# Optimization experiments

Measured on AMD Instinct MI355X. Metric: run time of the kernel, lower is better.

Reference implementation:

```python
import jax, jax.numpy as jnp
import numpy as np

N = 200000       # nodes
E = 6400000      # edges
F_IN, H1, H2, C = 7, 32, 16, 2


def gcn_conv(x, W, b, src, dst, n):
    """PyG GCNConv: add self-loops, symmetric normalization, linear, scatter-add."""
    loop = jnp.arange(n, dtype=src.dtype)
    s = jnp.concatenate([src, loop])
    d = jnp.concatenate([dst, loop])
    # degree of target nodes (with self-loops)
    deg = jax.ops.segment_sum(jnp.ones_like(d, dtype=x.dtype), d, num_segments=n)
    dinv = jnp.where(deg > 0, jax.lax.rsqrt(deg), 0.0)
    h = x @ W                                  # [n, out]
    norm = dinv[s] * dinv[d]                   # [e+n]
    msg = h[s] * norm[:, None]                 # gather + normalize
    out = jax.ops.segment_sum(msg, d, num_segments=n)  # scatter-add aggregation
    return out + b


def setup_inputs() -> dict:
    key = jax.random.key(0)
    ks = jax.random.split(key, 8)
    x = jax.random.normal(ks[0], (N, F_IN), dtype=jnp.float32)
    edge_index = jax.random.randint(ks[1], (2, E), 0, N, dtype=jnp.int64)
    def glorot(k, fan_in, fan_out):
        lim = np.sqrt(6.0 / (fan_in + fan_out)).astype(np.float32)
        return jax.random.uniform(k, (fan_in, fan_out), jnp.float32, -lim, lim)
    return {
        "x": x,
        "edge_index": edge_index,
        "W1": glorot(ks[2], F_IN, H1), "b1": jnp.zeros((H1,), jnp.float32),
        "W2": glorot(ks[3], H1, H2), "b2": jnp.zeros((H2,), jnp.float32),
        "Wfc": glorot(ks[4], H2, C), "bfc": jnp.zeros((C,), jnp.float32),
    }


def reference(x, edge_index, W1, b1, W2, b2, Wfc, bfc):
    src, dst = edge_index[0], edge_index[1]
    h = jax.nn.relu(gcn_conv(x, W1, b1, src, dst, N))
    h = jax.nn.relu(gcn_conv(h, W2, b2, src, dst, N))
    return h @ Wfc + bfc
```

## Files before the change

kernel.cpp:

```cpp
#include <hip/hip_runtime.h>

#define NNODES 200000
#define NEDGES 6400000
#define FIN 7
#define FH1 32
#define FH2 16
#define NC 2

#define WB 128
#define WB_SHIFT 7
#define NBUCK ((NNODES + WB - 1) / WB)
#define NBLK 512
#define CHUNK (NEDGES / NBLK)
#define PSHIFT 18
#define SRCMASK ((1u << PSHIFT) - 1)

#define RSTRIDE 4608
#define SCAP 5120


__global__ __launch_bounds__(256) void zero_cnt(int* __restrict__ cnt) {
    int i = blockIdx.x * 256 + threadIdx.x;
    if (i < NBUCK) cnt[i] = 0;
}


__global__ __launch_bounds__(256) void p2_sortres(const int* __restrict__ ei,
                                                  int* __restrict__ bucket_cur,
                                                  unsigned int* __restrict__ recs) {
    __shared__ int sorted[CHUNK];
    __shared__ int lcur[NBUCK];
    __shared__ int gbase[NBUCK];
    __shared__ int sm[256];
    int t = threadIdx.x;
    int blk = blockIdx.x;

    for (int i = t; i < NBUCK; i += 256) lcur[i] = 0;
    __syncthreads();

    int ebase = blk * CHUNK;
    for (int e = ebase + t; e < ebase + CHUNK; e += 256)
        atomicAdd(&lcur[ei[NEDGES + e] >> WB_SHIFT], 1);
    __syncthreads();

    int base7 = t * 7;
    int loc[7];
    int s = 0;
#pragma unroll
    for (int k = 0; k < 7; ++k) {
        int idx = base7 + k;
        int v = (idx < NBUCK) ? lcur[idx] : 0;
        loc[k] = v;
        s += v;
    }
    sm[t] = s;
    __syncthreads();
    for (int off = 1; off < 256; off <<= 1) {
        int v = (t >= off) ? sm[t - off] : 0;
        __syncthreads();
        sm[t] += v;
        __syncthreads();
    }
    int run = sm[t] - s;
#pragma unroll
    for (int k = 0; k < 7; ++k) {
        int idx = base7 + k;
        if (idx < NBUCK) { lcur[idx] = run; run += loc[k]; }
    }
    __syncthreads();

    for (int e = ebase + t; e < ebase + CHUNK; e += 256) {
        int src = ei[e];
        int d = ei[NEDGES + e];
        int b = d >> WB_SHIFT;
        int slot = atomicAdd(&lcur[b], 1);
        sorted[slot] = (int)((unsigned)src | ((unsigned)(d & (WB - 1)) << PSHIFT));
    }
    __syncthreads();

    for (int b = t; b < NBUCK; b += 256) {
        int st_ = (b > 0) ? lcur[b - 1] : 0;
        int len = lcur[b] - st_;
        if (len > 0)
            gbase[b] = b * RSTRIDE + atomicAdd(&bucket_cur[b], len);
    }
    __syncthreads();

    for (int i = t; i < CHUNK; i += 256) {
        int lo = 0, hi = NBUCK - 1;
        while (lo < hi) {
            int mid = (lo + hi) >> 1;
            if (lcur[mid] > i) hi = mid; else lo = mid + 1;
        }
        int b = lo;
        int start = (b > 0) ? lcur[b - 1] : 0;
        recs[(size_t)gbase[b] + (i - start)] = (unsigned)sorted[i];
    }
}


__global__ __launch_bounds__(256) void p2b_sort(unsigned int* __restrict__ recs,
                                                const int* __restrict__ bucket_cur,
                                                const float* __restrict__ x,
                                                int* __restrict__ node_off,
                                                float4* __restrict__ gx) {
    __shared__ int sorted[SCAP];
    __shared__ int hist[WB], st[WB], cur[WB];
    int t = threadIdx.x;
    int b = blockIdx.x;
    if (t < WB) hist[t] = 0;
    __syncthreads();

    int beg = b * RSTRIDE;
    int cnt = bucket_cur[b];

    for (int i = t; i < cnt; i += 256)
        atomicAdd(&hist[recs[(size_t)beg + i] >> PSHIFT], 1);
    __syncthreads();

    if (t < WB) cur[t] = hist[t];
    __syncthreads();
    for (int off = 1; off < WB; off <<= 1) {
        int v = 0;
        if (t < WB && t >= off) v = cur[t - off];
        __syncthreads();
        if (t < WB) cur[t] += v;
        __syncthreads();
    }
    if (t < WB) {
        st[t] = cur[t] - hist[t];
        cur[t] = st[t];
    }
    __syncthreads();

    for (int i = t; i < cnt; i += 256) {
        unsigned r = recs[(size_t)beg + i];
        int slot = atomicAdd(&cur[r >> PSHIFT], 1);
        sorted[slot] = (int)(r & SRCMASK);
    }
    __syncthreads();

    for (int i = t; i < cnt; i += 256)
        recs[(size_t)beg + i] = (unsigned)sorted[i];

    int node = b * WB + t;
    if (t < WB && node < NNODES) {
        node_off[node] = beg + st[t];
        float di = rsqrtf((float)(1 + hist[t]));
        const float* xr = x + (size_t)node * FIN;
        float4 v0, v1;
        v0.x = xr[0] * di; v0.y = xr[1] * di; v0.z = xr[2] * di; v0.w = xr[3] * di;
        v1.x = xr[4] * di; v1.y = xr[5] * di; v1.z = xr[6] * di; v1.w = 0.0f;
        gx[(size_t)node * 2 + 0] = v0;
        gx[(size_t)node * 2 + 1] = v1;
    }
}


__global__ __launch_bounds__(256) void l1_fast(const unsigned int* __restrict__ recs,
                                               const int* __restrict__ node_off,
                                               const int* __restrict__ bucket_cur,
                                               const float4* __restrict__ gx,
                                               const float* __restrict__ W1,
                                               const float* __restrict__ b1,
                                               const float* __restrict__ W2,
                                               float4* __restrict__ y) {
    __shared__ int sl_src[SCAP];
    __shared__ int noffs[WB + 1];
    __shared__ float acc[WB][9];
    __shared__ float sW1[FIN * FH1];
    __shared__ float sb1[FH1];
    __shared__ float sW2[FH1 * FH2];
    int t = threadIdx.x;
    for (int i = t; i < FIN * FH1; i += 256) sW1[i] = W1[i];
    if (t < FH1) sb1[t] = b1[t];
    for (int i = t; i < FH1 * FH2; i += 256) sW2[i] = W2[i];

    int b = blockIdx.x;
    int beg = b * RSTRIDE;
    int cnt_all = bucket_cur[b];
    for (int i = t; i < WB; i += 256) {
        int idx = b * WB + i;
        noffs[i] = (idx < NNODES) ? node_off[idx] : beg + cnt_all;
    }
    if (t == 0) noffs[WB] = beg + cnt_all;
    __syncthreads();

    for (int i = t; i < cnt_all; i += 256) sl_src[i] = (int)recs[(size_t)beg + i];
    __syncthreads();

    int n = t >> 1;
    int hq = t & 1;
    int base = noffs[n] - beg;
    int cnt = noffs[n + 1] - noffs[n];
    float ax = 0.0f, ay = 0.0f, az = 0.0f, aw = 0.0f;
    int k = 0;
    for (; k + 3 < cnt; k += 4) {
        int s0 = sl_src[base + k];
        int s1 = sl_src[base + k + 1];
        int s2 = sl_src[base + k + 2];
        int s3 = sl_src[base + k + 3];
        float4 v0 = gx[(size_t)s0 * 2 + hq];
        float4 v1 = gx[(size_t)s1 * 2 + hq];
        float4 v2 = gx[(size_t)s2 * 2 + hq];
        float4 v3 = gx[(size_t)s3 * 2 + hq];
        ax += v0.x + v1.x; ay += v0.y + v1.y;
        az += v0.z + v1.z; aw += v0.w + v1.w;
        ax += v2.x + v3.x; ay += v2.y + v3.y;
        az += v2.z + v3.z; aw += v2.w + v3.w;
    }
    for (; k < cnt; ++k) {
        int s0 = sl_src[base + k];
        float4 v0 = gx[(size_t)s0 * 2 + hq];
        ax += v0.x; ay += v0.y; az += v0.z; aw += v0.w;
    }
    int kb = hq * 4;
    acc[n][kb + 0] = ax; acc[n][kb + 1] = ay;
    acc[n][kb + 2] = az; acc[n][kb + 3] = aw;
    __syncthreads();

    int node = b * WB + t;
    if (t >= WB || node >= NNODES) return;

    float di = rsqrtf((float)(1 + (noffs[t + 1] - noffs[t])));
    float4 g0 = gx[(size_t)node * 2], g1 = gx[(size_t)node * 2 + 1];
    float xa[FIN];
    xa[0] = (acc[t][0] + g0.x) * di;
    xa[1] = (acc[t][1] + g0.y) * di;
    xa[2] = (acc[t][2] + g0.z) * di;
    xa[3] = (acc[t][3] + g0.w) * di;
    xa[4] = (acc[t][4] + g1.x) * di;
    xa[5] = (acc[t][5] + g1.y) * di;
    xa[6] = (acc[t][6] + g1.z) * di;

    float h1[FH1];
#pragma unroll
    for (int j = 0; j < FH1; ++j) h1[j] = sb1[j];
#pragma unroll
    for (int f = 0; f < FIN; ++f) {
        float xv = xa[f];
#pragma unroll
        for (int j = 0; j < FH1; ++j) h1[j] = fmaf(xv, sW1[f * FH1 + j], h1[j]);
    }
#pragma unroll
    for (int j = 0; j < FH1; ++j) h1[j] = fmaxf(h1[j], 0.0f);

    float yv[FH2];
#pragma unroll
    for (int j = 0; j < FH2; ++j) yv[j] = 0.0f;
#pragma unroll
    for (int k2 = 0; k2 < FH1; ++k2) {
        float hv = h1[k2];
#pragma unroll
        for (int j = 0; j < FH2; ++j) yv[j] = fmaf(hv, sW2[k2 * FH2 + j], yv[j]);
    }

    size_t yb = (size_t)node * 4;
    float4 o;
    o.x = yv[0] * di; o.y = yv[1] * di; o.z = yv[2] * di; o.w = yv[3] * di;
    y[yb + 0] = o;
    o.x = yv[4] * di; o.y = yv[5] * di; o.z = yv[6] * di; o.w = yv[7] * di;
    y[yb + 1] = o;
    o.x = yv[8] * di; o.y = yv[9] * di; o.z = yv[10] * di; o.w = yv[11] * di;
    y[yb + 2] = o;
    o.x = yv[12] * di; o.y = yv[13] * di; o.z = yv[14] * di; o.w = yv[15] * di;
    y[yb + 3] = o;
}


__global__ __launch_bounds__(256) void l2_fast(const unsigned int* __restrict__ recs,
                                               const int* __restrict__ node_off,
                                               const int* __restrict__ bucket_cur,
                                               const float4* __restrict__ y,
                                               const float* __restrict__ b2,
                                               const float* __restrict__ Wfc,
                                               const float* __restrict__ bfc,
                                               float2* __restrict__ out) {
    __shared__ int sl_src[SCAP];
    __shared__ int noffs[WB + 1];
    __shared__ float acc[WB][17];
    __shared__ float sb2[FH2];
    __shared__ float sWfc[FH2 * NC];
    __shared__ float sbfc[NC];
    int t = threadIdx.x;
    if (t < FH2) sb2[t] = b2[t];
    if (t < FH2 * NC) sWfc[t] = Wfc[t];
    if (t < NC) sbfc[t] = bfc[t];

    int b = blockIdx.x;
    int beg = b * RSTRIDE;
    int cnt_all = bucket_cur[b];
    for (int i = t; i < WB; i += 256) {
        int idx = b * WB + i;
        noffs[i] = (idx < NNODES) ? node_off[idx] : beg + cnt_all;
    }
    if (t == 0) noffs[WB] = beg + cnt_all;
    __syncthreads();

    for (int i = t; i < cnt_all; i += 256) sl_src[i] = (int)recs[(size_t)beg + i];
    __syncthreads();

    int q = t & 3;
#pragma unroll
    for (int r = 0; r < 2; ++r) {
        int n = (t >> 2) + 64 * r;
        int base = noffs[n] - beg;
        int cnt = noffs[n + 1] - noffs[n];
        float ax = 0.0f, ay = 0.0f, az = 0.0f, aw = 0.0f;
        int k = 0;
        for (; k + 3 < cnt; k += 4) {
            int s0 = sl_src[base + k];
            int s1 = sl_src[base + k + 1];
            int s2 = sl_src[base + k + 2];
            int s3 = sl_src[base + k + 3];
            float4 v0 = y[(size_t)s0 * 4 + q];
            float4 v1 = y[(size_t)s1 * 4 + q];
            float4 v2 = y[(size_t)s2 * 4 + q];
            float4 v3 = y[(size_t)s3 * 4 + q];
            ax += v0.x + v1.x; ay += v0.y + v1.y;
            az += v0.z + v1.z; aw += v0.w + v1.w;
            ax += v2.x + v3.x; ay += v2.y + v3.y;
            az += v2.z + v3.z; aw += v2.w + v3.w;
        }
        for (; k < cnt; ++k) {
            int s0 = sl_src[base + k];
            float4 v0 = y[(size_t)s0 * 4 + q];
            ax += v0.x; ay += v0.y; az += v0.z; aw += v0.w;
        }
        int kb = q * 4;
        acc[n][kb + 0] = ax; acc[n][kb + 1] = ay;
        acc[n][kb + 2] = az; acc[n][kb + 3] = aw;
    }
    __syncthreads();

    int node = b * WB + t;
    if (t >= WB || node >= NNODES) return;

    float di = rsqrtf((float)(1 + (noffs[t + 1] - noffs[t])));
    size_t yb = (size_t)node * 4;
    float4 s0 = y[yb + 0], s1 = y[yb + 1], s2 = y[yb + 2], s3 = y[yb + 3];
    float self[FH2] = {s0.x, s0.y, s0.z, s0.w, s1.x, s1.y, s1.z, s1.w,
                       s2.x, s2.y, s2.z, s2.w, s3.x, s3.y, s3.z, s3.w};

    float o0 = sbfc[0], o1 = sbfc[1];
#pragma unroll
    for (int k = 0; k < FH2; ++k) {
        float h = fmaxf(fmaf(di, acc[t][k] + self[k], sb2[k]), 0.0f);
        o0 = fmaf(h, sWfc[k * NC + 0], o0);
        o1 = fmaf(h, sWfc[k * NC + 1], o1);
    }
    float2 ov; ov.x = o0; ov.y = o1;
    out[node] = ov;
}


extern "C" void kernel_launch(void* const* d_in, const int* in_sizes, int n_in,
                              void* d_out, int out_size, void* d_ws, size_t ws_size,
                              hipStream_t stream) {
    const float* x   = (const float*)d_in[0];
    const int*   ei  = (const int*)d_in[1];
    const float* W1  = (const float*)d_in[2];
    const float* b1  = (const float*)d_in[3];
    const float* W2  = (const float*)d_in[4];
    const float* b2  = (const float*)d_in[5];
    const float* Wfc = (const float*)d_in[6];
    const float* bfc = (const float*)d_in[7];
    float* out = (float*)d_out;

    char* p = (char*)d_ws;
    auto carve = [&](size_t bytes) -> char* {
        char* r = p;
        p += (bytes + 255) & ~(size_t)255;
        return r;
    };
    int*      bucket_cur = (int*)carve((size_t)NBUCK * 4);
    int*      node_off   = (int*)carve((size_t)NNODES * 4);
    float*    gx         = (float*)carve((size_t)NNODES * 8 * 4);
    float*    y          = (float*)carve((size_t)NNODES * 16 * 4);
    unsigned* recs       = (unsigned*)carve((size_t)NBUCK * RSTRIDE * 4);

    zero_cnt<<<(NBUCK + 255) / 256, 256, 0, stream>>>(bucket_cur);
    p2_sortres<<<NBLK, 256, 0, stream>>>(ei, bucket_cur, recs);
    p2b_sort<<<NBUCK, 256, 0, stream>>>(recs, bucket_cur, x, node_off, (float4*)gx);
    l1_fast<<<NBUCK, 256, 0, stream>>>(recs, node_off, bucket_cur, (const float4*)gx,
                                       W1, b1, W2, (float4*)y);
    l2_fast<<<NBUCK, 256, 0, stream>>>(recs, node_off, bucket_cur, (const float4*)y,
                                       b2, Wfc, bfc, (float2*)out);
}
```

Measured before the change: 347.3 us.

## Single-pass register-cached counting sort and deeper gather unroll

Both bucketing kernels now read each edge record once, keep the packed value and its atomic rank in registers, and scatter using prefix offsets plus rank. This removes the second global read pass and the second round of shared atomics. The first kernel doubles its block count to shrink per-block chunks, and folds the global bucket reservation into the scan loop. The aggregation gather loops unroll by 8 for more memory-level parallelism, which raises register pressure and may lower occupancy.

```diff
diff --git a/kernel.cpp b/kernel.cpp
--- a/kernel.cpp
+++ b/kernel.cpp
@@ -10,12 +10,14 @@
 #define WB 128
 #define WB_SHIFT 7
 #define NBUCK ((NNODES + WB - 1) / WB)
-#define NBLK 512
+#define NBLK 1024
 #define CHUNK (NEDGES / NBLK)
+#define EPT ((CHUNK + 255) / 256)
 #define PSHIFT 18
 #define SRCMASK ((1u << PSHIFT) - 1)
 
 #define RSTRIDE 4608
+#define BPT ((RSTRIDE + 255) / 256)
 #define SCAP 5120
 
 
@@ -39,8 +41,21 @@
     __syncthreads();
 
     int ebase = blk * CHUNK;
-    for (int e = ebase + t; e < ebase + CHUNK; e += 256)
-        atomicAdd(&lcur[ei[NEDGES + e] >> WB_SHIFT], 1);
+    int es[EPT];
+    int rb[EPT];
+#pragma unroll
+    for (int j = 0; j < EPT; ++j) {
+        int idx = j * 256 + t;
+        if (idx < CHUNK) {
+            int e = ebase + idx;
+            int src = ei[e];
+            int d = ei[NEDGES + e];
+            int b = d >> WB_SHIFT;
+            int rank = atomicAdd(&lcur[b], 1);
+            es[j] = (int)((unsigned)src | ((unsigned)(d & (WB - 1)) << PSHIFT));
+            rb[j] = (b << 16) | rank;
+        }
+    }
     __syncthreads();
 
     int base7 = t * 7;
@@ -65,36 +80,34 @@
 #pragma unroll
     for (int k = 0; k < 7; ++k) {
         int idx = base7 + k;
-        if (idx < NBUCK) { lcur[idx] = run; run += loc[k]; }
-    }
-    __syncthreads();
-
-    for (int e = ebase + t; e < ebase + CHUNK; e += 256) {
-        int src = ei[e];
-        int d = ei[NEDGES + e];
-        int b = d >> WB_SHIFT;
-        int slot = atomicAdd(&lcur[b], 1);
-        sorted[slot] = (int)((unsigned)src | ((unsigned)(d & (WB - 1)) << PSHIFT));
-    }
-    __syncthreads();
-
-    for (int b = t; b < NBUCK; b += 256) {
-        int st_ = (b > 0) ? lcur[b - 1] : 0;
-        int len = lcur[b] - st_;
-        if (len > 0)
-            gbase[b] = b * RSTRIDE + atomicAdd(&bucket_cur[b], len);
+        if (idx < NBUCK) {
+            lcur[idx] = run;
+            if (loc[k] > 0)
+                gbase[idx] = idx * RSTRIDE + atomicAdd(&bucket_cur[idx], loc[k]);
+            run += loc[k];
+        }
+    }
+    __syncthreads();
+
+#pragma unroll
+    for (int j = 0; j < EPT; ++j) {
+        int idx = j * 256 + t;
+        if (idx < CHUNK) {
+            int b = rb[j] >> 16;
+            int rank = rb[j] & 0xffff;
+            sorted[lcur[b] + rank] = es[j];
+        }
     }
     __syncthreads();
 
     for (int i = t; i < CHUNK; i += 256) {
         int lo = 0, hi = NBUCK - 1;
         while (lo < hi) {
-            int mid = (lo + hi) >> 1;
-            if (lcur[mid] > i) hi = mid; else lo = mid + 1;
+            int mid = (lo + hi + 1) >> 1;
+            if (lcur[mid] <= i) lo = mid; else hi = mid - 1;
         }
         int b = lo;
-        int start = (b > 0) ? lcur[b - 1] : 0;
-        recs[(size_t)gbase[b] + (i - start)] = (unsigned)sorted[i];
+        recs[(size_t)gbase[b] + (i - lcur[b])] = (unsigned)sorted[i];
     }
 }
 
@@ -105,7 +118,7 @@
                                                 int* __restrict__ node_off,
                                                 float4* __restrict__ gx) {
     __shared__ int sorted[SCAP];
-    __shared__ int hist[WB], st[WB], cur[WB];
+    __shared__ int hist[WB], st[WB];
     int t = threadIdx.x;
     int b = blockIdx.x;
     if (t < WB) hist[t] = 0;
@@ -114,29 +127,41 @@
     int beg = b * RSTRIDE;
     int cnt = bucket_cur[b];
 
-    for (int i = t; i < cnt; i += 256)
-        atomicAdd(&hist[recs[(size_t)beg + i] >> PSHIFT], 1);
-    __syncthreads();
-
-    if (t < WB) cur[t] = hist[t];
+    int es[BPT];
+    int rr[BPT];
+#pragma unroll
+    for (int j = 0; j < BPT; ++j) {
+        int i = j * 256 + t;
+        if (i < cnt) {
+            unsigned r = recs[(size_t)beg + i];
+            int dl = r >> PSHIFT;
+            int rank = atomicAdd(&hist[dl], 1);
+            es[j] = (int)(r & SRCMASK);
+            rr[j] = dl | (rank << 7);
+        }
+    }
+    __syncthreads();
+
+    if (t < WB) st[t] = hist[t];
     __syncthreads();
     for (int off = 1; off < WB; off <<= 1) {
         int v = 0;
-        if (t < WB && t >= off) v = cur[t - off];
+        if (t < WB && t >= off) v = st[t - off];
         __syncthreads();
-        if (t < WB) cur[t] += v;
+        if (t < WB) st[t] += v;
         __syncthreads();
     }
-    if (t < WB) {
-        st[t] = cur[t] - hist[t];
-        cur[t] = st[t];
-    }
-    __syncthreads();
-
-    for (int i = t; i < cnt; i += 256) {
-        unsigned r = recs[(size_t)beg + i];
-        int slot = atomicAdd(&cur[r >> PSHIFT], 1);
-        sorted[slot] = (int)(r & SRCMASK);
+    if (t < WB) st[t] -= hist[t];
+    __syncthreads();
+
+#pragma unroll
+    for (int j = 0; j < BPT; ++j) {
+        int i = j * 256 + t;
+        if (i < cnt) {
+            int dl = rr[j] & (WB - 1);
+            int rank = rr[j] >> 7;
+            sorted[st[dl] + rank] = es[j];
+        }
     }
     __syncthreads();
 
@@ -195,19 +220,31 @@
     int cnt = noffs[n + 1] - noffs[n];
     float ax = 0.0f, ay = 0.0f, az = 0.0f, aw = 0.0f;
     int k = 0;
-    for (; k + 3 < cnt; k += 4) {
+    for (; k + 7 < cnt; k += 8) {
         int s0 = sl_src[base + k];
         int s1 = sl_src[base + k + 1];
         int s2 = sl_src[base + k + 2];
         int s3 = sl_src[base + k + 3];
+        int s4 = sl_src[base + k + 4];
+        int s5 = sl_src[base + k + 5];
+        int s6 = sl_src[base + k + 6];
+        int s7 = sl_src[base + k + 7];
         float4 v0 = gx[(size_t)s0 * 2 + hq];
         float4 v1 = gx[(size_t)s1 * 2 + hq];
         float4 v2 = gx[(size_t)s2 * 2 + hq];
         float4 v3 = gx[(size_t)s3 * 2 + hq];
+        float4 v4 = gx[(size_t)s4 * 2 + hq];
+        float4 v5 = gx[(size_t)s5 * 2 + hq];
+        float4 v6 = gx[(size_t)s6 * 2 + hq];
+        float4 v7 = gx[(size_t)s7 * 2 + hq];
         ax += v0.x + v1.x; ay += v0.y + v1.y;
         az += v0.z + v1.z; aw += v0.w + v1.w;
         ax += v2.x + v3.x; ay += v2.y + v3.y;
         az += v2.z + v3.z; aw += v2.w + v3.w;
+        ax += v4.x + v5.x; ay += v4.y + v5.y;
+        az += v4.z + v5.z; aw += v4.w + v5.w;
+        ax += v6.x + v7.x; ay += v6.y + v7.y;
+        az += v6.z + v7.z; aw += v6.w + v7.w;
     }
     for (; k < cnt; ++k) {
         int s0 = sl_src[base + k];
@@ -308,19 +345,31 @@
         int cnt = noffs[n + 1] - noffs[n];
         float ax = 0.0f, ay = 0.0f, az = 0.0f, aw = 0.0f;
         int k = 0;
-        for (; k + 3 < cnt; k += 4) {
+        for (; k + 7 < cnt; k += 8) {
             int s0 = sl_src[base + k];
             int s1 = sl_src[base + k + 1];
             int s2 = sl_src[base + k + 2];
             int s3 = sl_src[base + k + 3];
+            int s4 = sl_src[base + k + 4];
+            int s5 = sl_src[base + k + 5];
+            int s6 = sl_src[base + k + 6];
+            int s7 = sl_src[base + k + 7];
             float4 v0 = y[(size_t)s0 * 4 + q];
             float4 v1 = y[(size_t)s1 * 4 + q];
             float4 v2 = y[(size_t)s2 * 4 + q];
             float4 v3 = y[(size_t)s3 * 4 + q];
+            float4 v4 = y[(size_t)s4 * 4 + q];
+            float4 v5 = y[(size_t)s5 * 4 + q];
+            float4 v6 = y[(size_t)s6 * 4 + q];
+            float4 v7 = y[(size_t)s7 * 4 + q];
             ax += v0.x + v1.x; ay += v0.y + v1.y;
             az += v0.z + v1.z; aw += v0.w + v1.w;
             ax += v2.x + v3.x; ay += v2.y + v3.y;
             az += v2.z + v3.z; aw += v2.w + v3.w;
+            ax += v4.x + v5.x; ay += v4.y + v5.y;
+            az += v4.z + v5.z; aw += v4.w + v5.w;
+            ax += v6.x + v7.x; ay += v6.y + v7.y;
+            az += v6.z + v7.z; aw += v6.w + v7.w;
         }
         for (; k < cnt; ++k) {
             int s0 = sl_src[base + k];
```

Measured after the change: 427.8 us. 23.2% more time.
